# Optimization experiments

Hardware: AMD Instinct MI355X
Metric: run time of the kernel (lower is better)

The kernel has to match this reference:

```python
import jax, jax.numpy as jnp
import numpy as np

LEAKY_ALPHA = 0.2  # tf.nn.leaky_relu default

N_NODES = 65536
N_EDGES = 1048576
D = 64


def setup_inputs() -> dict:
    key = jax.random.key(0)
    k1, k2, k3, k4 = jax.random.split(key, 4)
    x = jax.random.normal(k1, (N_NODES, D), dtype=jnp.float32)
    edge_index = jax.random.randint(k2, (2, N_EDGES), 0, N_NODES, dtype=jnp.int64)
    W1 = jax.random.normal(k3, (D, D), dtype=jnp.float32) * 0.05
    b1 = jnp.zeros((D,), dtype=jnp.float32)
    W2 = jax.random.normal(k4, (D, D), dtype=jnp.float32) * 0.05
    b2 = jnp.zeros((D,), dtype=jnp.float32)
    return {"x": x, "edge_index": edge_index, "W1": W1, "b1": b1, "W2": W2, "b2": b2}


def _leaky_relu(v):
    return jnp.where(v >= 0, v, LEAKY_ALPHA * v)


def reference(x, edge_index, W1, b1, W2, b2):
    n = x.shape[0]
    src = edge_index[0]
    dst = edge_index[1]
    # LightGCN symmetric normalization: w_e = deg[src]^-1/2 * deg[dst]^-1/2
    ones = jnp.ones(src.shape, dtype=x.dtype)
    deg = jax.ops.segment_sum(ones, dst, num_segments=n)
    inv_sqrt = jnp.where(deg > 0, jax.lax.rsqrt(jnp.maximum(deg, 1.0)), 0.0)
    w = inv_sqrt[src] * inv_sqrt[dst]  # [E]
    # SpMM: h = normed_adj @ x  (gather + weighted scatter-add)
    h = jax.ops.segment_sum(x[src] * w[:, None], dst, num_segments=n)  # [N, D]
    # dual dense transform + elementwise gate
    out = _leaky_relu(h @ W1 + b1) + _leaky_relu((x * h) @ W2 + b2)
    return out
```

## Files before the change

kernel.cpp:

```cpp
#include <hip/hip_runtime.h>

#define N_NODES 65536
#define N_EDGES 1048576
#define D 64
#define NB 256
#define CHUNK (N_EDGES / NB)
#define SSTAGE 6144
#define FBCAP 65536

typedef __bf16 bf16x8 __attribute__((ext_vector_type(8)));
typedef float f32x4 __attribute__((ext_vector_type(4)));

__device__ __forceinline__ int edge_at(const void* ei, int is64, long long pos) {
    if (is64) return (int)((const long long*)ei)[pos];
    return ((const int*)ei)[pos];
}

__device__ __forceinline__ int detect_is64(const unsigned* ei, int* s_is64) {
    if (threadIdx.x < 64) {
        unsigned v = ei[2 * threadIdx.x + 1];
        unsigned long long nz = __ballot(v != 0u);
        if (threadIdx.x == 0) *s_is64 = (nz == 0ull) ? 1 : 0;
    }
    __syncthreads();
    return *s_is64;
}

__global__ __launch_bounds__(256) void passA_kernel(const void* ei,
                                                    unsigned* __restrict__ H,
                                                    unsigned* __restrict__ L,
                                                    unsigned* __restrict__ pairs_cs) {
    __shared__ unsigned ed[CHUNK];
    __shared__ unsigned srt[CHUNK];
    __shared__ unsigned hist[NB];
    __shared__ unsigned scn[NB];
    __shared__ int s_is64;
    const int is64 = detect_is64((const unsigned*)ei, &s_is64);
    const int t = threadIdx.x;
    const int w = blockIdx.x;
    hist[t] = 0;
    __syncthreads();
    const int base = w * CHUNK;
    for (int i = t; i < CHUNK; i += 256) {
        unsigned src = (unsigned)edge_at(ei, is64, base + i);
        unsigned dst = (unsigned)edge_at(ei, is64, (long long)N_EDGES + base + i);
        ed[i] = src | (dst << 16);
        atomicAdd(&hist[dst >> 8], 1u);
    }
    __syncthreads();
    const unsigned own = hist[t];
    scn[t] = own;
    __syncthreads();
    for (int off = 1; off < NB; off <<= 1) {
        unsigned v = (t >= off) ? scn[t - off] : 0u;
        __syncthreads();
        scn[t] += v;
        __syncthreads();
    }
    const unsigned excl = scn[t] - own;
    H[t * NB + w] = own;
    L[t * NB + w] = excl;
    hist[t] = excl;
    __syncthreads();
    for (int i = t; i < CHUNK; i += 256) {
        unsigned p = ed[i];
        unsigned pos = atomicAdd(&hist[p >> 24], 1u);
        srt[pos] = p;
    }
    __syncthreads();
    for (int i = t; i < CHUNK; i += 256) pairs_cs[(size_t)w * CHUNK + i] = srt[i];
}

__global__ __launch_bounds__(256) void scanT_kernel(const unsigned* __restrict__ H,
                                                    unsigned* __restrict__ bucket_start) {
    __shared__ unsigned cs[NB];
    const int t = threadIdx.x;
    const uint4* Hr = (const uint4*)(H + t * NB);
    unsigned tot = 0;
#pragma unroll 8
    for (int k = 0; k < NB / 4; ++k) {
        uint4 q = Hr[k];
        tot += q.x + q.y + q.z + q.w;
    }
    const unsigned own = tot;
    cs[t] = own;
    __syncthreads();
    for (int off = 1; off < NB; off <<= 1) {
        unsigned v = (t >= off) ? cs[t - off] : 0u;
        __syncthreads();
        cs[t] += v;
        __syncthreads();
    }
    bucket_start[t] = cs[t] - own;
    if (t == NB - 1) bucket_start[NB] = cs[t];
}

__global__ __launch_bounds__(256) void bucketB_kernel(const unsigned* __restrict__ pairs_cs,
                                                      const unsigned* __restrict__ H,
                                                      const unsigned* __restrict__ L,
                                                      const unsigned* __restrict__ bucket_start,
                                                      const float* __restrict__ x,
                                                      unsigned* __restrict__ row_start,
                                                      unsigned short* __restrict__ src16,
                                                      unsigned* __restrict__ y32,
                                                      unsigned* __restrict__ fb) {
    __shared__ unsigned s_pairs[SSTAGE];
    __shared__ unsigned short s_src[SSTAGE];
    __shared__ unsigned hist[NB];
    __shared__ unsigned scn[NB];
    __shared__ unsigned degs[NB];
    const int t = threadIdx.x;
    const int b = blockIdx.x;
    const unsigned base = bucket_start[b];
    const unsigned cnt = bucket_start[b + 1] - base;
    const bool staged = (cnt <= SSTAGE);

    const unsigned Hb = H[b * NB + t];
    const unsigned Lb = L[b * NB + t];
    scn[t] = Hb;
    __syncthreads();
    for (int off = 1; off < NB; off <<= 1) {
        unsigned v = (t >= off) ? scn[t - off] : 0u;
        __syncthreads();
        scn[t] += v;
        __syncthreads();
    }
    const unsigned ex = scn[t] - Hb;
    unsigned* wp = staged ? s_pairs : (fb + (size_t)b * FBCAP);
    for (unsigned j = 0; j < Hb; ++j) wp[ex + j] = pairs_cs[(size_t)t * CHUNK + Lb + j];
    __syncthreads();
    const unsigned* pp = staged ? s_pairs : (fb + (size_t)b * FBCAP);

    hist[t] = 0;
    __syncthreads();
    for (unsigned i = t; i < cnt; i += 256u) {
        atomicAdd(&hist[(pp[i] >> 16) & 255u], 1u);
    }
    __syncthreads();
    const unsigned own = hist[t];
    degs[t] = own;
    scn[t] = own;
    __syncthreads();
    for (int off = 1; off < NB; off <<= 1) {
        unsigned v = (t >= off) ? scn[t - off] : 0u;
        __syncthreads();
        scn[t] += v;
        __syncthreads();
    }
    const unsigned excl = scn[t] - own;
    row_start[b * NB + t] = base + excl;
    if (b == NB - 1 && t == 0) row_start[N_NODES] = N_EDGES;
    hist[t] = excl;
    __syncthreads();
    if (staged) {
        for (unsigned i = t; i < cnt; i += 256u) {
            unsigned p = pp[i];
            unsigned pos = atomicAdd(&hist[(p >> 16) & 255u], 1u);
            s_src[pos] = (unsigned short)(p & 0xFFFFu);
        }
        __syncthreads();
        for (unsigned i = t; i < cnt; i += 256u) src16[base + i] = s_src[i];
    } else {
        for (unsigned i = t; i < cnt; i += 256u) {
            unsigned p = pp[i];
            unsigned pos = atomicAdd(&hist[(p >> 16) & 255u], 1u);
            src16[base + pos] = (unsigned short)(p & 0xFFFFu);
        }
    }
    const int nbase = b * NB;
    for (int idx = t; idx < NB * 32; idx += 256) {
        int nl = idx >> 5;
        int c = (idx & 31) * 2;
        unsigned d = degs[nl];
        float w = d ? rsqrtf((float)d) : 0.f;
        float2 v = *(const float2*)(x + (nbase + nl) * D + c);
        unsigned lo = (unsigned)__builtin_bit_cast(unsigned short, (__bf16)(v.x * w));
        unsigned hi = (unsigned)__builtin_bit_cast(unsigned short, (__bf16)(v.y * w));
        y32[(nbase + nl) * 32 + (idx & 31)] = lo | (hi << 16);
    }
}

#define BLO(u) __uint_as_float((u) << 16)
#define BHI(u) __uint_as_float((u) & 0xffff0000u)
__device__ __forceinline__ unsigned pkbf(float lo, float hi) {
    return (unsigned)__builtin_bit_cast(unsigned short, (__bf16)lo) |
           ((unsigned)__builtin_bit_cast(unsigned short, (__bf16)hi) << 16);
}
__global__ __launch_bounds__(256) void spmm_kernel(const unsigned short* __restrict__ src16,
                                                   const unsigned* __restrict__ row_start,
                                                   const uint4* __restrict__ y128,
                                                   uint4* __restrict__ hb4) {
    const int lane = threadIdx.x & 63;
    const int grp = lane >> 3;
    const int r8 = lane & 7;
    int wid = (blockIdx.x * blockDim.x + threadIdx.x) >> 6;
    int nw = (gridDim.x * blockDim.x) >> 6;
    for (int n = wid; n < N_NODES; n += nw) {
        const unsigned start = row_start[n];
        const unsigned end = row_start[n + 1];
        float a0 = 0.f, a1 = 0.f, a2 = 0.f, a3 = 0.f;
        float a4 = 0.f, a5 = 0.f, a6 = 0.f, a7 = 0.f;
        float c0 = 0.f, c1 = 0.f, c2 = 0.f, c3 = 0.f;
        float c4 = 0.f, c5 = 0.f, c6 = 0.f, c7 = 0.f;
        unsigned i = start;
        for (; i + 16 <= end; i += 16) {
            int sA = (int)src16[i + grp];
            int sB = (int)src16[i + 8 + grp];
            uint4 pA = y128[sA * 8 + r8];
            uint4 pB = y128[sB * 8 + r8];
            a0 += BLO(pA.x); a1 += BHI(pA.x);
            a2 += BLO(pA.y); a3 += BHI(pA.y);
            a4 += BLO(pA.z); a5 += BHI(pA.z);
            a6 += BLO(pA.w); a7 += BHI(pA.w);
            c0 += BLO(pB.x); c1 += BHI(pB.x);
            c2 += BLO(pB.y); c3 += BHI(pB.y);
            c4 += BLO(pB.z); c5 += BHI(pB.z);
            c6 += BLO(pB.w); c7 += BHI(pB.w);
        }
        for (; i < end; i += 8) {
            if (i + grp < end) {
                int s = (int)src16[i + grp];
                uint4 p = y128[s * 8 + r8];
                a0 += BLO(p.x); a1 += BHI(p.x);
                a2 += BLO(p.y); a3 += BHI(p.y);
                a4 += BLO(p.z); a5 += BHI(p.z);
                a6 += BLO(p.w); a7 += BHI(p.w);
            }
        }
        a0 += c0; a1 += c1; a2 += c2; a3 += c3;
        a4 += c4; a5 += c5; a6 += c6; a7 += c7;
        a0 += __shfl_xor(a0, 8); a0 += __shfl_xor(a0, 16); a0 += __shfl_xor(a0, 32);
        a1 += __shfl_xor(a1, 8); a1 += __shfl_xor(a1, 16); a1 += __shfl_xor(a1, 32);
        a2 += __shfl_xor(a2, 8); a2 += __shfl_xor(a2, 16); a2 += __shfl_xor(a2, 32);
        a3 += __shfl_xor(a3, 8); a3 += __shfl_xor(a3, 16); a3 += __shfl_xor(a3, 32);
        a4 += __shfl_xor(a4, 8); a4 += __shfl_xor(a4, 16); a4 += __shfl_xor(a4, 32);
        a5 += __shfl_xor(a5, 8); a5 += __shfl_xor(a5, 16); a5 += __shfl_xor(a5, 32);
        a6 += __shfl_xor(a6, 8); a6 += __shfl_xor(a6, 16); a6 += __shfl_xor(a6, 32);
        a7 += __shfl_xor(a7, 8); a7 += __shfl_xor(a7, 16); a7 += __shfl_xor(a7, 32);
        const float w = (end > start) ? rsqrtf((float)(end - start)) : 0.f;
        if (grp == 0) {
            uint4 v;
            v.x = pkbf(a0 * w, a1 * w);
            v.y = pkbf(a2 * w, a3 * w);
            v.z = pkbf(a4 * w, a5 * w);
            v.w = pkbf(a6 * w, a7 * w);
            hb4[n * 8 + r8] = v;
        }
    }
}

__global__ __launch_bounds__(256) void dense_mfma_kernel(const float* __restrict__ x,
                                                         const uint4* __restrict__ hb4,
                                                         const float* __restrict__ W1,
                                                         const float* __restrict__ b1,
                                                         const float* __restrict__ W2,
                                                         const float* __restrict__ b2,
                                                         float* __restrict__ out) {
    const int lane = threadIdx.x & 63;
    const int lo = lane & 15;
    const int hi = lane >> 4;

    bf16x8 bw1[2][4], bw2[2][4];
#pragma unroll
    for (int kt = 0; kt < 2; ++kt)
#pragma unroll
        for (int nt = 0; nt < 4; ++nt) {
            bf16x8 v1, v2;
#pragma unroll
            for (int j = 0; j < 8; ++j) {
                int k = kt * 32 + hi * 8 + j;
                int n = nt * 16 + lo;
                v1[j] = (__bf16)W1[k * D + n];
                v2[j] = (__bf16)W2[k * D + n];
            }
            bw1[kt][nt] = v1;
            bw2[kt][nt] = v2;
        }
    float bb1[4], bb2[4];
#pragma unroll
    for (int nt = 0; nt < 4; ++nt) {
        bb1[nt] = b1[nt * 16 + lo];
        bb2[nt] = b2[nt * 16 + lo];
    }

    int wid = (blockIdx.x * blockDim.x + threadIdx.x) >> 6;
    int nw = (gridDim.x * blockDim.x) >> 6;
    for (int blk = wid; blk < N_NODES / 16; blk += nw) {
        const int rb = blk * 16;
        const uint4* hrow = hb4 + (rb + lo) * 8;
        const float* xrow = x + (rb + lo) * D;
        bf16x8 ah[2], ag[2];
#pragma unroll
        for (int kt = 0; kt < 2; ++kt) {
            const int c = kt * 32 + hi * 8;
            uint4 hp = hrow[kt * 4 + hi];
            float4 xv0 = *(const float4*)(xrow + c);
            float4 xv1 = *(const float4*)(xrow + c + 4);
            ah[kt] = __builtin_bit_cast(bf16x8, hp);
            bf16x8 g;
            g[0] = (__bf16)(BLO(hp.x) * xv0.x);
            g[1] = (__bf16)(BHI(hp.x) * xv0.y);
            g[2] = (__bf16)(BLO(hp.y) * xv0.z);
            g[3] = (__bf16)(BHI(hp.y) * xv0.w);
            g[4] = (__bf16)(BLO(hp.z) * xv1.x);
            g[5] = (__bf16)(BHI(hp.z) * xv1.y);
            g[6] = (__bf16)(BLO(hp.w) * xv1.z);
            g[7] = (__bf16)(BHI(hp.w) * xv1.w);
            ag[kt] = g;
        }
        f32x4 acc1[4], acc2[4];
#pragma unroll
        for (int nt = 0; nt < 4; ++nt) {
            acc1[nt] = (f32x4){0.f, 0.f, 0.f, 0.f};
            acc2[nt] = (f32x4){0.f, 0.f, 0.f, 0.f};
        }
#pragma unroll
        for (int kt = 0; kt < 2; ++kt)
#pragma unroll
            for (int nt = 0; nt < 4; ++nt) {
                acc1[nt] = __builtin_amdgcn_mfma_f32_16x16x32_bf16(ah[kt], bw1[kt][nt], acc1[nt], 0, 0, 0);
                acc2[nt] = __builtin_amdgcn_mfma_f32_16x16x32_bf16(ag[kt], bw2[kt][nt], acc2[nt], 0, 0, 0);
            }
#pragma unroll
        for (int nt = 0; nt < 4; ++nt)
#pragma unroll
            for (int r = 0; r < 4; ++r) {
                float a1 = acc1[nt][r] + bb1[nt];
                float a2 = acc2[nt][r] + bb2[nt];
                a1 = (a1 >= 0.f) ? a1 : 0.2f * a1;
                a2 = (a2 >= 0.f) ? a2 : 0.2f * a2;
                out[(rb + hi * 4 + r) * D + nt * 16 + lo] = a1 + a2;
            }
    }
}

extern "C" void kernel_launch(void* const* d_in, const int* in_sizes, int n_in,
                              void* d_out, int out_size, void* d_ws, size_t ws_size,
                              hipStream_t stream) {
    const float* x  = (const float*)d_in[0];
    const void*  ei = d_in[1];
    const float* W1 = (const float*)d_in[2];
    const float* b1 = (const float*)d_in[3];
    const float* W2 = (const float*)d_in[4];
    const float* b2 = (const float*)d_in[5];
    float* out = (float*)d_out;

    char* p = (char*)d_ws;
    unsigned* bucket_start = (unsigned*)p;       p += 4096;
    unsigned* row_start    = (unsigned*)p;       p += 266240;
    unsigned* H            = (unsigned*)p;       p += NB * NB * 4;
    unsigned* L            = (unsigned*)p;       p += NB * NB * 4;
    unsigned short* src16  = (unsigned short*)p; p += (size_t)N_EDGES * 2;
    unsigned* y32          = (unsigned*)p;       p += (size_t)N_NODES * 32 * 4;
    unsigned* hb           = (unsigned*)p;       p += (size_t)N_NODES * 32 * 4;
    unsigned* fb           = (unsigned*)p;

    unsigned* pairs_cs = (unsigned*)d_out;

    passA_kernel<<<NB, 256, 0, stream>>>(ei, H, L, pairs_cs);
    scanT_kernel<<<1, 256, 0, stream>>>(H, bucket_start);
    bucketB_kernel<<<NB, 256, 0, stream>>>(pairs_cs, H, L, bucket_start, x,
                                           row_start, src16, y32, fb);
    spmm_kernel<<<4096, 256, 0, stream>>>(src16, row_start, (const uint4*)y32, (uint4*)hb);
    dense_mfma_kernel<<<1024, 256, 0, stream>>>(x, (const uint4*)hb, W1, b1, W2, b2, out);
}
```

Baseline: 82.89 us.

## Split gathered features into column planes and drop separate scan kernel

The bf16 feature table y32 and the SpMM output hb are stored as four 16-column planes instead of row-major 64-column rows. SpMM blocks are assigned to one plane each, so every gathered row is a 32-byte fragment and each plane's working set (1 MB) is more likely to stay in cache. Each node is now processed four times across planes with narrower lanes. Separately, the single-block scanT kernel is replaced by atomic totals in passA plus a memset, with every bucketB block redoing the 256-entry scan. This costs an extra memset launch and redundant scan work per block.

```diff
diff --git a/kernel.cpp b/kernel.cpp
--- a/kernel.cpp
+++ b/kernel.cpp
@@ -7,6 +7,7 @@
 #define CHUNK (N_EDGES / NB)
 #define SSTAGE 6144
 #define FBCAP 65536
+#define PLANEU (N_NODES * 8)
 
 typedef __bf16 bf16x8 __attribute__((ext_vector_type(8)));
 typedef float f32x4 __attribute__((ext_vector_type(4)));
@@ -29,6 +30,7 @@
 __global__ __launch_bounds__(256) void passA_kernel(const void* ei,
                                                     unsigned* __restrict__ H,
                                                     unsigned* __restrict__ L,
+                                                    unsigned* __restrict__ tot,
                                                     unsigned* __restrict__ pairs_cs) {
     __shared__ unsigned ed[CHUNK];
     __shared__ unsigned srt[CHUNK];
@@ -60,6 +62,7 @@
     const unsigned excl = scn[t] - own;
     H[t * NB + w] = own;
     L[t * NB + w] = excl;
+    atomicAdd(&tot[t], own);
     hist[t] = excl;
     __syncthreads();
     for (int i = t; i < CHUNK; i += 256) {
@@ -71,34 +74,10 @@
     for (int i = t; i < CHUNK; i += 256) pairs_cs[(size_t)w * CHUNK + i] = srt[i];
 }
 
-__global__ __launch_bounds__(256) void scanT_kernel(const unsigned* __restrict__ H,
-                                                    unsigned* __restrict__ bucket_start) {
-    __shared__ unsigned cs[NB];
-    const int t = threadIdx.x;
-    const uint4* Hr = (const uint4*)(H + t * NB);
-    unsigned tot = 0;
-#pragma unroll 8
-    for (int k = 0; k < NB / 4; ++k) {
-        uint4 q = Hr[k];
-        tot += q.x + q.y + q.z + q.w;
-    }
-    const unsigned own = tot;
-    cs[t] = own;
-    __syncthreads();
-    for (int off = 1; off < NB; off <<= 1) {
-        unsigned v = (t >= off) ? cs[t - off] : 0u;
-        __syncthreads();
-        cs[t] += v;
-        __syncthreads();
-    }
-    bucket_start[t] = cs[t] - own;
-    if (t == NB - 1) bucket_start[NB] = cs[t];
-}
-
 __global__ __launch_bounds__(256) void bucketB_kernel(const unsigned* __restrict__ pairs_cs,
                                                       const unsigned* __restrict__ H,
                                                       const unsigned* __restrict__ L,
-                                                      const unsigned* __restrict__ bucket_start,
+                                                      const unsigned* __restrict__ tot,
                                                       const float* __restrict__ x,
                                                       unsigned* __restrict__ row_start,
                                                       unsigned short* __restrict__ src16,
@@ -109,11 +88,23 @@
     __shared__ unsigned hist[NB];
     __shared__ unsigned scn[NB];
     __shared__ unsigned degs[NB];
+    __shared__ unsigned s_tot[NB];
     const int t = threadIdx.x;
     const int b = blockIdx.x;
-    const unsigned base = bucket_start[b];
-    const unsigned cnt = bucket_start[b + 1] - base;
+
+    s_tot[t] = tot[t];
+    scn[t] = s_tot[t];
+    __syncthreads();
+    for (int off = 1; off < NB; off <<= 1) {
+        unsigned v = (t >= off) ? scn[t - off] : 0u;
+        __syncthreads();
+        scn[t] += v;
+        __syncthreads();
+    }
+    const unsigned base = scn[b] - s_tot[b];
+    const unsigned cnt = s_tot[b];
     const bool staged = (cnt <= SSTAGE);
+    __syncthreads();
 
     const unsigned Hb = H[b * NB + t];
     const unsigned Lb = L[b * NB + t];
@@ -170,13 +161,14 @@
     const int nbase = b * NB;
     for (int idx = t; idx < NB * 32; idx += 256) {
         int nl = idx >> 5;
-        int c = (idx & 31) * 2;
+        int col = idx & 31;
         unsigned d = degs[nl];
         float w = d ? rsqrtf((float)d) : 0.f;
-        float2 v = *(const float2*)(x + (nbase + nl) * D + c);
+        float2 v = *(const float2*)(x + (nbase + nl) * D + col * 2);
         unsigned lo = (unsigned)__builtin_bit_cast(unsigned short, (__bf16)(v.x * w));
         unsigned hi = (unsigned)__builtin_bit_cast(unsigned short, (__bf16)(v.y * w));
-        y32[(nbase + nl) * 32 + (idx & 31)] = lo | (hi << 16);
+        y32[(size_t)(col >> 3) * PLANEU + (size_t)(nbase + nl) * 8 + (col & 7)] =
+            lo | (hi << 16);
     }
 }
 
@@ -188,69 +180,47 @@
 }
 __global__ __launch_bounds__(256) void spmm_kernel(const unsigned short* __restrict__ src16,
                                                    const unsigned* __restrict__ row_start,
-                                                   const uint4* __restrict__ y128,
-                                                   uint4* __restrict__ hb4) {
+                                                   const unsigned* __restrict__ y32,
+                                                   unsigned* __restrict__ hb) {
     const int lane = threadIdx.x & 63;
-    const int grp = lane >> 3;
-    const int r8 = lane & 7;
-    int wid = (blockIdx.x * blockDim.x + threadIdx.x) >> 6;
-    int nw = (gridDim.x * blockDim.x) >> 6;
+    const int wv = threadIdx.x >> 6;
+    const int grp = lane >> 2;
+    const int r4 = lane & 3;
+    const int q = (blockIdx.x & 7) >> 1;
+    const unsigned* yq = y32 + (size_t)q * PLANEU;
+    unsigned* hq = hb + (size_t)q * PLANEU;
+    const int rank = ((blockIdx.x >> 3) << 1) | (blockIdx.x & 1);
+    const int nw = (int)(gridDim.x >> 1);
+    int wid = rank * 4 + wv;
     for (int n = wid; n < N_NODES; n += nw) {
         const unsigned start = row_start[n];
         const unsigned end = row_start[n + 1];
         float a0 = 0.f, a1 = 0.f, a2 = 0.f, a3 = 0.f;
-        float a4 = 0.f, a5 = 0.f, a6 = 0.f, a7 = 0.f;
-        float c0 = 0.f, c1 = 0.f, c2 = 0.f, c3 = 0.f;
-        float c4 = 0.f, c5 = 0.f, c6 = 0.f, c7 = 0.f;
-        unsigned i = start;
-        for (; i + 16 <= end; i += 16) {
-            int sA = (int)src16[i + grp];
-            int sB = (int)src16[i + 8 + grp];
-            uint4 pA = y128[sA * 8 + r8];
-            uint4 pB = y128[sB * 8 + r8];
-            a0 += BLO(pA.x); a1 += BHI(pA.x);
-            a2 += BLO(pA.y); a3 += BHI(pA.y);
-            a4 += BLO(pA.z); a5 += BHI(pA.z);
-            a6 += BLO(pA.w); a7 += BHI(pA.w);
-            c0 += BLO(pB.x); c1 += BHI(pB.x);
-            c2 += BLO(pB.y); c3 += BHI(pB.y);
-            c4 += BLO(pB.z); c5 += BHI(pB.z);
-            c6 += BLO(pB.w); c7 += BHI(pB.w);
-        }
-        for (; i < end; i += 8) {
-            if (i + grp < end) {
-                int s = (int)src16[i + grp];
-                uint4 p = y128[s * 8 + r8];
+        for (unsigned i = start; i < end; i += 16u) {
+            unsigned idx = i + grp;
+            if (idx < end) {
+                int s = (int)src16[idx];
+                uint2 p = *(const uint2*)(yq + s * 8 + r4 * 2);
                 a0 += BLO(p.x); a1 += BHI(p.x);
                 a2 += BLO(p.y); a3 += BHI(p.y);
-                a4 += BLO(p.z); a5 += BHI(p.z);
-                a6 += BLO(p.w); a7 += BHI(p.w);
             }
         }
-        a0 += c0; a1 += c1; a2 += c2; a3 += c3;
-        a4 += c4; a5 += c5; a6 += c6; a7 += c7;
-        a0 += __shfl_xor(a0, 8); a0 += __shfl_xor(a0, 16); a0 += __shfl_xor(a0, 32);
-        a1 += __shfl_xor(a1, 8); a1 += __shfl_xor(a1, 16); a1 += __shfl_xor(a1, 32);
-        a2 += __shfl_xor(a2, 8); a2 += __shfl_xor(a2, 16); a2 += __shfl_xor(a2, 32);
-        a3 += __shfl_xor(a3, 8); a3 += __shfl_xor(a3, 16); a3 += __shfl_xor(a3, 32);
-        a4 += __shfl_xor(a4, 8); a4 += __shfl_xor(a4, 16); a4 += __shfl_xor(a4, 32);
-        a5 += __shfl_xor(a5, 8); a5 += __shfl_xor(a5, 16); a5 += __shfl_xor(a5, 32);
-        a6 += __shfl_xor(a6, 8); a6 += __shfl_xor(a6, 16); a6 += __shfl_xor(a6, 32);
-        a7 += __shfl_xor(a7, 8); a7 += __shfl_xor(a7, 16); a7 += __shfl_xor(a7, 32);
+        a0 += __shfl_xor(a0, 4); a0 += __shfl_xor(a0, 8); a0 += __shfl_xor(a0, 16); a0 += __shfl_xor(a0, 32);
+        a1 += __shfl_xor(a1, 4); a1 += __shfl_xor(a1, 8); a1 += __shfl_xor(a1, 16); a1 += __shfl_xor(a1, 32);
+        a2 += __shfl_xor(a2, 4); a2 += __shfl_xor(a2, 8); a2 += __shfl_xor(a2, 16); a2 += __shfl_xor(a2, 32);
+        a3 += __shfl_xor(a3, 4); a3 += __shfl_xor(a3, 8); a3 += __shfl_xor(a3, 16); a3 += __shfl_xor(a3, 32);
         const float w = (end > start) ? rsqrtf((float)(end - start)) : 0.f;
         if (grp == 0) {
-            uint4 v;
+            uint2 v;
             v.x = pkbf(a0 * w, a1 * w);
             v.y = pkbf(a2 * w, a3 * w);
-            v.z = pkbf(a4 * w, a5 * w);
-            v.w = pkbf(a6 * w, a7 * w);
-            hb4[n * 8 + r8] = v;
+            *(uint2*)(hq + (size_t)n * 8 + r4 * 2) = v;
         }
     }
 }
 
 __global__ __launch_bounds__(256) void dense_mfma_kernel(const float* __restrict__ x,
-                                                         const uint4* __restrict__ hb4,
+                                                         const unsigned* __restrict__ hb,
                                                          const float* __restrict__ W1,
                                                          const float* __restrict__ b1,
                                                          const float* __restrict__ W2,
@@ -287,13 +257,14 @@
     int nw = (gridDim.x * blockDim.x) >> 6;
     for (int blk = wid; blk < N_NODES / 16; blk += nw) {
         const int rb = blk * 16;
-        const uint4* hrow = hb4 + (rb + lo) * 8;
+        const unsigned* hrowu = hb + (size_t)(rb + lo) * 8 + (hi & 1) * 4;
         const float* xrow = x + (rb + lo) * D;
         bf16x8 ah[2], ag[2];
 #pragma unroll
         for (int kt = 0; kt < 2; ++kt) {
             const int c = kt * 32 + hi * 8;
-            uint4 hp = hrow[kt * 4 + hi];
+            const int q = kt * 2 + (hi >> 1);
+            uint4 hp = *(const uint4*)(hrowu + (size_t)q * PLANEU);
             float4 xv0 = *(const float4*)(xrow + c);
             float4 xv1 = *(const float4*)(xrow + c + 4);
             ah[kt] = __builtin_bit_cast(bf16x8, hp);
@@ -346,21 +317,21 @@
     float* out = (float*)d_out;
 
     char* p = (char*)d_ws;
-    unsigned* bucket_start = (unsigned*)p;       p += 4096;
+    unsigned* tot          = (unsigned*)p;       p += 4096;
     unsigned* row_start    = (unsigned*)p;       p += 266240;
     unsigned* H            = (unsigned*)p;       p += NB * NB * 4;
     unsigned* L            = (unsigned*)p;       p += NB * NB * 4;
     unsigned short* src16  = (unsigned short*)p; p += (size_t)N_EDGES * 2;
-    unsigned* y32          = (unsigned*)p;       p += (size_t)N_NODES * 32 * 4;
-    unsigned* hb           = (unsigned*)p;       p += (size_t)N_NODES * 32 * 4;
+    unsigned* y32          = (unsigned*)p;       p += (size_t)4 * PLANEU * 4;
+    unsigned* hb           = (unsigned*)p;       p += (size_t)4 * PLANEU * 4;
     unsigned* fb           = (unsigned*)p;
 
     unsigned* pairs_cs = (unsigned*)d_out;
 
-    passA_kernel<<<NB, 256, 0, stream>>>(ei, H, L, pairs_cs);
-    scanT_kernel<<<1, 256, 0, stream>>>(H, bucket_start);
-    bucketB_kernel<<<NB, 256, 0, stream>>>(pairs_cs, H, L, bucket_start, x,
+    hipMemsetAsync(tot, 0, NB * sizeof(unsigned), stream);
+    passA_kernel<<<NB, 256, 0, stream>>>(ei, H, L, tot, pairs_cs);
+    bucketB_kernel<<<NB, 256, 0, stream>>>(pairs_cs, H, L, tot, x,
                                            row_start, src16, y32, fb);
-    spmm_kernel<<<4096, 256, 0, stream>>>(src16, row_start, (const uint4*)y32, (uint4*)hb);
-    dense_mfma_kernel<<<1024, 256, 0, stream>>>(x, (const uint4*)hb, W1, b1, W2, b2, out);
-}
+    spmm_kernel<<<4096, 256, 0, stream>>>(src16, row_start, y32, hb);
+    dense_mfma_kernel<<<1024, 256, 0, stream>>>(x, hb, W1, b1, W2, b2, out);
+}
```

Measured after the change: 161.4 us. 94.7% more time.
